# Kernel optimization log

Measured on AMD Instinct MI355X. Metric: run time of the kernel, lower is better.

## Reference

```python
import jax, jax.numpy as jnp
import numpy as np

N = 50000     # num_nodes
E = 600000    # num_edges
H = 128       # h_dim
OUT = 32      # out_dim
R = 64        # num_rels
B = 16        # num_bases


def setup_inputs() -> dict:
    key = jax.random.key(0)
    ks = jax.random.split(key, 11)
    src = jax.random.randint(ks[0], (E,), 0, N)
    dst = jax.random.randint(ks[1], (E,), 0, N)
    etype = jax.random.randint(ks[2], (E,), 0, R)
    norm = jax.random.uniform(ks[3], (E, 1), dtype=jnp.float32)  # edge norm (e.g. 1/deg)
    emb = jax.random.normal(ks[4], (N, H), dtype=jnp.float32) * 0.05
    # basis-decomposed relation weights: W_r = sum_b comp[r,b] * V[b]
    V1 = jax.random.normal(ks[5], (B, H, H), dtype=jnp.float32) * (1.0 / np.sqrt(H))
    comp1 = jax.random.normal(ks[6], (R, B), dtype=jnp.float32) * (1.0 / np.sqrt(B))
    bias1 = jnp.zeros((H,), dtype=jnp.float32)
    V2 = jax.random.normal(ks[7], (B, H, OUT), dtype=jnp.float32) * (1.0 / np.sqrt(H))
    comp2 = jax.random.normal(ks[8], (R, B), dtype=jnp.float32) * (1.0 / np.sqrt(B))
    bias2 = jnp.zeros((OUT,), dtype=jnp.float32)
    return {"src": src, "dst": dst, "etype": etype, "norm": norm, "emb": emb,
            "V1": V1, "comp1": comp1, "bias1": bias1,
            "V2": V2, "comp2": comp2, "bias2": bias2}


def _rel_graph_conv(x, src, dst, etype, norm, V, comp, bias):
    # message for edge e: (x[src_e] @ W_{etype_e}) * norm_e, W_r = sum_b comp[r,b] V_b.
    # Since W is linear, fold norm into the gathered features, and aggregate
    # per (dst, basis) BEFORE the dense basis matmul (aggregate-first trick):
    #   agg[v, b] = sum_{e: dst_e=v} comp[etype_e, b] * norm_e * x[src_e]
    #   out[v]    = sum_b agg[v, b] @ V_b + bias
    xs = x[src] * norm                      # [E, in]
    w = comp[etype]                         # [E, B] per-edge basis coefficients
    # loop over the small fixed basis count (B=16), reusing the [E, in] buffer
    agg = jnp.stack(
        [jax.ops.segment_sum(xs * w[:, b:b + 1], dst, num_segments=N) for b in range(B)],
        axis=1,
    )                                       # [N, B, in]
    return jnp.einsum('nbi,bio->no', agg, V) + bias


def reference(src, dst, etype, norm, emb, V1, comp1, bias1, V2, comp2, bias2):
    h = _rel_graph_conv(emb, src, dst, etype, norm, V1, comp1, bias1)
    h = jax.nn.relu(h)                      # dropout p=0.0 -> identity
    h = _rel_graph_conv(h, src, dst, etype, norm, V2, comp2, bias2)
    return h
```

## Files before the change

### kernel.cpp

```cpp
#include <hip/hip_runtime.h>
#include <hip/hip_bf16.h>

#define NN 50000
#define EE 600000
#define HH 128
#define OUTD 32
#define RR 64
#define BB 16
#define KK 2048
#define SC_B ((NN + 1023) / 1024)

typedef short s16x8 __attribute__((ext_vector_type(8)));
typedef float f32x4 __attribute__((ext_vector_type(4)));
typedef float f32x2 __attribute__((ext_vector_type(2)));
typedef unsigned short ushort_t;
typedef unsigned int uint_t;
typedef __attribute__((address_space(3))) uint_t lds_u32;
typedef const __attribute__((address_space(1))) uint_t glb_u32;

__device__ inline ushort_t f_to_bf16(float f){
    __hip_bfloat16 h = __float2bfloat16(f);
    return *reinterpret_cast<ushort_t*>(&h);
}
__device__ inline uint_t pack_bf16x2(float a, float b){
    return (uint_t)f_to_bf16(a) | ((uint_t)f_to_bf16(b) << 16);
}

__global__ void zero_i32(int* p, int n){
    int i = blockIdx.x*256 + threadIdx.x;
    if (i < n) p[i] = 0;
}

__global__ void hist_kernel(const int* __restrict__ dst, int* counts){
    int e = blockIdx.x*256 + threadIdx.x;
    if (e < EE) atomicAdd(&counts[dst[e]], 1);
}

__global__ void scan_part(const int* __restrict__ counts, int* __restrict__ tot){
    int b = blockIdx.x, t = threadIdx.x;
    int i0 = b*1024 + t*4;
    int s = 0;
    if (i0 + 3 < NN){
        int4 v = *reinterpret_cast<const int4*>(&counts[i0]);
        s = v.x + v.y + v.z + v.w;
    } else {
        for (int j = 0; j < 4; j++) if (i0 + j < NN) s += counts[i0 + j];
    }
    #pragma unroll
    for (int off = 32; off; off >>= 1) s += __shfl_xor(s, off, 64);
    __shared__ int ws[4];
    if ((t & 63) == 0) ws[t >> 6] = s;
    __syncthreads();
    if (t == 0) tot[b] = ws[0] + ws[1] + ws[2] + ws[3];
}

__global__ void scan_tot(int* tot){
    int t = threadIdx.x;
    int v = (t < SC_B) ? tot[t] : 0;
    int x = v;
    #pragma unroll
    for (int off = 1; off < 64; off <<= 1){
        int y = __shfl_up(x, off, 64);
        if (t >= off) x += y;
    }
    if (t < SC_B) tot[t] = x - v;
}

__global__ void scan_final(const int* __restrict__ counts, const int* __restrict__ tot,
                           int* __restrict__ offsets, int* __restrict__ cursor){
    int b = blockIdx.x, t = threadIdx.x, lane = t & 63, wv = t >> 6;
    int i0 = b*1024 + t*4;
    int v[4]; int s = 0;
    #pragma unroll
    for (int j = 0; j < 4; j++){ v[j] = (i0 + j < NN) ? counts[i0 + j] : 0; s += v[j]; }
    int x = s;
    #pragma unroll
    for (int off = 1; off < 64; off <<= 1){
        int y = __shfl_up(x, off, 64);
        if (lane >= off) x += y;
    }
    __shared__ int ws[4];
    if (lane == 63) ws[wv] = x;
    __syncthreads();
    int pre = tot[b];
    for (int i = 0; i < wv; i++) pre += ws[i];
    int run = pre + x - s;
    #pragma unroll
    for (int j = 0; j < 4; j++){
        if (i0 + j < NN){
            cursor[i0 + j] = run;
            offsets[i0 + j + 1] = run + v[j];
        }
        run += v[j];
    }
    if (b == 0 && t == 0) offsets[0] = 0;
}

__global__ void scatter_kernel(const int* __restrict__ dst, const int* __restrict__ src,
                               const int* __restrict__ etype, const float* __restrict__ norm,
                               int* cursor, int* __restrict__ msrc, int* __restrict__ netn){
    int e = blockIdx.x*256 + threadIdx.x;
    if (e >= EE) return;
    int d = dst[e];
    int r = atomicAdd(&cursor[d], 1);
    msrc[r] = src[e];
    netn[r] = (__float_as_int(norm[e]) & ~63) | etype[e];
}

__global__ void convw_kernel(const float* __restrict__ V1, const float* __restrict__ V2,
                             ushort_t* __restrict__ Wt1, ushort_t* __restrict__ Wt2){
    int i = blockIdx.x*256 + threadIdx.x;
    if (i < HH*KK){
        int o = i / KK, k = i % KK;
        Wt1[i] = f_to_bf16(V1[(size_t)k*HH + o]);
    } else {
        int j = i - HH*KK;
        if (j < OUTD*KK){
            int o = j / KK, k = j % KK;
            Wt2[j] = f_to_bf16(V2[(size_t)k*OUTD + o]);
        }
    }
}

__global__ void conv_emb(const float* __restrict__ emb, ushort_t* __restrict__ xb){
    int i = blockIdx.x*256 + threadIdx.x;
    if (i < NN*HH/2){
        float2 f = *reinterpret_cast<const float2*>(emb + 2*(size_t)i);
        *reinterpret_cast<uint_t*>(xb + 2*(size_t)i) = pack_bf16x2(f.x, f.y);
    }
}

__global__ __launch_bounds__(256, 8) void agg_kernel(
    const ushort_t* __restrict__ xin, const int* __restrict__ msrc,
    const int* __restrict__ netn, const int* __restrict__ offsets,
    const float* __restrict__ comp, ushort_t* __restrict__ agg,
    int v0, int vc)
{
    int w = threadIdx.x >> 6, lane = threadIdx.x & 63;
    int v = v0 + blockIdx.x*4 + w;
    if (v >= v0 + vc) return;
    int p0 = offsets[v];
    int dd = offsets[v+1] - p0;
    const uint_t* xrow = reinterpret_cast<const uint_t*>(xin);

    f32x2 accA[8], accB[8];
    #pragma unroll
    for (int bp = 0; bp < 8; bp++){
        accA[bp].x = 0.f; accA[bp].y = 0.f;
        accB[bp].x = 0.f; accB[bp].y = 0.f;
    }

    for (int c0 = 0; c0 < dd; c0 += 64){
        int nc = min(64, dd - c0);
        int li = p0 + c0 + min(lane, nc - 1);
        int mp = msrc[li];
        int nr = netn[li];
        uint_t xr[8];
        #pragma unroll
        for (int j = 0; j < 8; ++j){
            int sr = __builtin_amdgcn_readlane(mp, min(j, nc - 1));
            xr[j] = xrow[(size_t)sr*64 + lane];
        }
        for (int eb = 0; eb < nc; eb += 8){
            #pragma unroll
            for (int j = 0; j < 8; ++j){
                int e = eb + j;
                int ec = min(e, nc - 1);
                int nb = __builtin_amdgcn_readlane(nr, ec);
                int et = nb & 63;
                float nw = (e < nc) ? __int_as_float(nb & ~63) : 0.f;
                uint_t u = xr[j];
                f32x2 xs;
                xs.x = __uint_as_float(u << 16) * nw;
                xs.y = __uint_as_float(u & 0xffff0000u) * nw;
                int en = e + 8;
                if (en < nc){
                    int srn = __builtin_amdgcn_readlane(mp, en);
                    xr[j] = xrow[(size_t)srn*64 + lane];
                }
                const f32x2* cp = reinterpret_cast<const f32x2*>(comp + et*BB);
                #pragma unroll
                for (int bp = 0; bp < 8; bp++){
                    f32x2 c2 = cp[bp];
                    asm("v_pk_fma_f32 %0, %1, %2, %0 op_sel:[0,0,0] op_sel_hi:[1,0,1]"
                        : "+v"(accA[bp]) : "s"(c2), "v"(xs));
                    asm("v_pk_fma_f32 %0, %1, %2, %0 op_sel:[0,1,0] op_sel_hi:[1,1,1]"
                        : "+v"(accB[bp]) : "s"(c2), "v"(xs));
                }
            }
        }
    }
    uint_t* arow = reinterpret_cast<uint_t*>(agg) + (size_t)(v - v0)*1024 + lane;
    #pragma unroll
    for (int b = 0; b < BB; b++)
        arow[b*64] = pack_bf16x2(accA[b>>1][b&1], accB[b>>1][b&1]);
}

template<int BN, bool RELU, bool OUT_BF16>
__global__ __launch_bounds__(512, 4) void gemm_kernel(
    const ushort_t* __restrict__ A, const ushort_t* __restrict__ Wt,
    const float* __restrict__ bias, void* __restrict__ yout, int vc)
{
    __shared__ __align__(16) char Ald[2][128*128];
    __shared__ __align__(16) char Bld[2][BN*128];
    constexpr int RT = (BN == 128) ? 2 : 1;
    constexpr int CT = (BN == 128) ? 4 : 2;
    constexpr int NT = KK / 64;
    int tid = threadIdx.x, lane = tid & 63, lane15 = lane & 15;
    int w = tid >> 6;
    int wrbase = (BN == 128) ? (w >> 1)*32 : w*16;
    int wcbase = (BN == 128) ? (w & 1)*64 : 0;
    int m0 = blockIdx.x * 128;

    int rl = lane >> 3, jl = lane & 7;
    int ra0 = w*2*8 + rl,  ra1 = (w*2+1)*8 + rl;
    const ushort_t* agp0 = A + (size_t)(m0 + min(ra0, vc-1))*KK + ((jl ^ (ra0 & 7))*8);
    const ushort_t* agp1 = A + (size_t)(m0 + min(ra1, vc-1))*KK + ((jl ^ (ra1 & 7))*8);
    const ushort_t* bgp0;
    const ushort_t* bgp1;
    if (BN == 128){
        bgp0 = Wt + (size_t)ra0*KK + ((jl ^ (ra0 & 7))*8);
        bgp1 = Wt + (size_t)ra1*KK + ((jl ^ (ra1 & 7))*8);
    } else {
        int rb = w*8 + rl;
        bgp0 = Wt + (size_t)min(rb, BN-1)*KK + ((jl ^ (rb & 7))*8);
        bgp1 = nullptr;
    }

    auto stage = [&](int buf){
        __builtin_amdgcn_global_load_lds((glb_u32*)agp0,
            (lds_u32*)(&Ald[buf][(w*2+0)*1024]), 16, 0, 0);
        __builtin_amdgcn_global_load_lds((glb_u32*)agp1,
            (lds_u32*)(&Ald[buf][(w*2+1)*1024]), 16, 0, 0);
        agp0 += 64; agp1 += 64;
        if constexpr (BN == 128){
            __builtin_amdgcn_global_load_lds((glb_u32*)bgp0,
                (lds_u32*)(&Bld[buf][(w*2+0)*1024]), 16, 0, 0);
            __builtin_amdgcn_global_load_lds((glb_u32*)bgp1,
                (lds_u32*)(&Bld[buf][(w*2+1)*1024]), 16, 0, 0);
            bgp0 += 64; bgp1 += 64;
        } else {
            if (w < 4){
                __builtin_amdgcn_global_load_lds((glb_u32*)bgp0,
                    (lds_u32*)(&Bld[buf][w*1024]), 16, 0, 0);
                bgp0 += 64;
            }
        }
    };

    f32x4 acc[RT][CT];
    #pragma unroll
    for (int t = 0; t < RT; t++)
        #pragma unroll
        for (int ct = 0; ct < CT; ct++)
            #pragma unroll
            for (int j = 0; j < 4; j++) acc[t][ct][j] = 0.f;

    auto compute = [&](int buf){
        #pragma unroll
        for (int ks = 0; ks < 2; ks++){
            int csw = (ks*4 + (lane >> 4)) ^ (lane15 & 7);
            #pragma unroll
            for (int t = 0; t < RT; t++){
                int arow = wrbase + t*16 + lane15;
                s16x8 a = *reinterpret_cast<const s16x8*>(&Ald[buf][arow*128 + csw*16]);
                #pragma unroll
                for (int ct = 0; ct < CT; ct++){
                    int brow = wcbase + ct*16 + lane15;
                    s16x8 b = *reinterpret_cast<const s16x8*>(&Bld[buf][brow*128 + csw*16]);
                    acc[t][ct] = __builtin_amdgcn_mfma_f32_16x16x32_bf16(a, b, acc[t][ct], 0,0,0);
                }
            }
        }
    };

    stage(0);
    for (int t = 0; t < NT; ++t){
        int cur = t & 1;
        if (t + 1 < NT){
            stage(cur ^ 1);
            if (BN == 128)       asm volatile("s_waitcnt vmcnt(4)" ::: "memory");
            else if (w < 4)      asm volatile("s_waitcnt vmcnt(3)" ::: "memory");
            else                 asm volatile("s_waitcnt vmcnt(2)" ::: "memory");
        } else {
            asm volatile("s_waitcnt vmcnt(0)" ::: "memory");
        }
        __builtin_amdgcn_s_barrier();
        __builtin_amdgcn_sched_barrier(0);
        compute(cur);
        __builtin_amdgcn_s_barrier();
    }

    #pragma unroll
    for (int t = 0; t < RT; t++){
        int rb = m0 + wrbase + t*16 + ((lane >> 4) << 2);
        #pragma unroll
        for (int ct = 0; ct < CT; ct++){
            int col = wcbase + ct*16 + lane15;
            float bv = bias[col];
            #pragma unroll
            for (int r = 0; r < 4; r++){
                int row = rb + r;
                if (row < vc){
                    float val = acc[t][ct][r] + bv;
                    if (RELU) val = fmaxf(val, 0.f);
                    if (OUT_BF16)
                        reinterpret_cast<ushort_t*>(yout)[(size_t)row*BN + col] = f_to_bf16(val);
                    else
                        reinterpret_cast<float*>(yout)[(size_t)row*BN + col] = val;
                }
            }
        }
    }
}

extern "C" void kernel_launch(void* const* d_in, const int* in_sizes, int n_in,
                              void* d_out, int out_size, void* d_ws, size_t ws_size,
                              hipStream_t stream){
    const int*   src   = (const int*)d_in[0];
    const int*   dst   = (const int*)d_in[1];
    const int*   etype = (const int*)d_in[2];
    const float* norm  = (const float*)d_in[3];
    const float* emb   = (const float*)d_in[4];
    const float* V1    = (const float*)d_in[5];
    const float* comp1 = (const float*)d_in[6];
    const float* bias1 = (const float*)d_in[7];
    const float* V2    = (const float*)d_in[8];
    const float* comp2 = (const float*)d_in[9];
    const float* bias2 = (const float*)d_in[10];
    float* out = (float*)d_out;

    char* w = (char*)d_ws;
    auto alloc = [&](size_t bytes) -> char* {
        char* p = w; w += (bytes + 255) & ~(size_t)255; return p;
    };
    int*      offsets = (int*)alloc((NN + 1) * 4);
    int*      counts  = (int*)alloc(NN * 4);
    int*      cursor  = (int*)alloc(NN * 4);
    int*      tot     = (int*)alloc(SC_B * 4);
    int*      msrc    = (int*)alloc((size_t)EE * 4);
    int*      netn    = (int*)alloc((size_t)EE * 4);
    ushort_t* Wt1     = (ushort_t*)alloc((size_t)HH * KK * 2);
    ushort_t* Wt2     = (ushort_t*)alloc((size_t)OUTD * KK * 2);
    ushort_t* xb      = (ushort_t*)alloc((size_t)NN * HH * 2);
    ushort_t* h       = (ushort_t*)alloc((size_t)NN * HH * 2);
    size_t used  = (size_t)(w - (char*)d_ws);
    size_t avail = ws_size > used ? ws_size - used : 0;
    int chunkN = (int)(avail / ((size_t)KK * 2));
    chunkN &= ~127;
    if (chunkN < 128) chunkN = 128;
    if (chunkN > NN) chunkN = NN;
    ushort_t* agg = (ushort_t*)w;

    zero_i32<<<(NN + 255)/256, 256, 0, stream>>>(counts, NN);
    hist_kernel<<<(EE + 255)/256, 256, 0, stream>>>(dst, counts);
    scan_part<<<SC_B, 256, 0, stream>>>(counts, tot);
    scan_tot<<<1, 64, 0, stream>>>(tot);
    scan_final<<<SC_B, 256, 0, stream>>>(counts, tot, offsets, cursor);
    scatter_kernel<<<(EE + 255)/256, 256, 0, stream>>>(dst, src, etype, norm,
                                                       cursor, msrc, netn);
    convw_kernel<<<((HH + OUTD)*KK + 255)/256, 256, 0, stream>>>(V1, V2, Wt1, Wt2);
    conv_emb<<<(NN*HH/2 + 255)/256, 256, 0, stream>>>(emb, xb);

    for (int v0 = 0; v0 < NN; v0 += chunkN){
        int vc = (NN - v0 < chunkN) ? (NN - v0) : chunkN;
        agg_kernel<<<(vc + 3)/4, 256, 0, stream>>>(
            xb, msrc, netn, offsets, comp1, agg, v0, vc);
        gemm_kernel<HH, true, true><<<(vc + 127)/128, 512, 0, stream>>>(
            agg, Wt1, bias1, h + (size_t)v0 * HH, vc);
    }
    for (int v0 = 0; v0 < NN; v0 += chunkN){
        int vc = (NN - v0 < chunkN) ? (NN - v0) : chunkN;
        agg_kernel<<<(vc + 3)/4, 256, 0, stream>>>(
            h, msrc, netn, offsets, comp2, agg, v0, vc);
        gemm_kernel<OUTD, false, false><<<(vc + 127)/128, 512, 0, stream>>>(
            agg, Wt2, bias2, out + (size_t)v0 * OUTD, vc);
    }
}
```

Baseline: 310.1 us.

## Precompute per-edge norm-scaled basis coefficients and fuse prep kernels

Adds a per-edge array wedge[E,16] holding comp[etype]*norm, built in a fused prep kernel for layer 1 and by a separate kernel for layer 2. The aggregation kernel then reads these coefficients directly, dropping the per-edge readlane decode, the etype lookup and the norm multiply, and splits off a tail loop for the last partial group of 8 edges. It also merges the weight and embedding conversion launches into one kernel and replaces the zeroing kernel with hipMemsetAsync. The cost is about 38 MB of extra writes per layer and 64 bytes of coefficient reads per edge instead of a 4-byte packed word.

```diff
diff --git a/kernel.cpp b/kernel.cpp
--- a/kernel.cpp
+++ b/kernel.cpp
@@ -9,6 +9,8 @@
 #define BB 16
 #define KK 2048
 #define SC_B ((NN + 1023) / 1024)
+#define N_CONVW ((HH + OUTD) * KK)
+#define N_EMB   (NN * HH / 2)
 
 typedef short s16x8 __attribute__((ext_vector_type(8)));
 typedef float f32x4 __attribute__((ext_vector_type(4)));
@@ -24,11 +26,6 @@
 }
 __device__ inline uint_t pack_bf16x2(float a, float b){
     return (uint_t)f_to_bf16(a) | ((uint_t)f_to_bf16(b) << 16);
-}
-
-__global__ void zero_i32(int* p, int n){
-    int i = blockIdx.x*256 + threadIdx.x;
-    if (i < n) p[i] = 0;
 }
 
 __global__ void hist_kernel(const int* __restrict__ dst, int* counts){
@@ -107,34 +104,54 @@
     netn[r] = (__float_as_int(norm[e]) & ~63) | etype[e];
 }
 
-__global__ void convw_kernel(const float* __restrict__ V1, const float* __restrict__ V2,
-                             ushort_t* __restrict__ Wt1, ushort_t* __restrict__ Wt2){
+__device__ inline void build_w_one(int e, const int* __restrict__ netn,
+                                   const float* __restrict__ comp,
+                                   float* __restrict__ wedge){
+    int nb = netn[e];
+    int et = nb & 63;
+    float nw = __int_as_float(nb & ~63);
+    const float4* c = reinterpret_cast<const float4*>(comp + et*BB);
+    float4* wp = reinterpret_cast<float4*>(wedge + (size_t)e*BB);
+    #pragma unroll
+    for (int q = 0; q < 4; q++){
+        float4 cv = c[q];
+        wp[q] = make_float4(cv.x*nw, cv.y*nw, cv.z*nw, cv.w*nw);
+    }
+}
+
+__global__ void build_w_kernel(const int* __restrict__ netn, const float* __restrict__ comp,
+                               float* __restrict__ wedge){
+    int e = blockIdx.x*256 + threadIdx.x;
+    if (e < EE) build_w_one(e, netn, comp, wedge);
+}
+
+__global__ void prep_kernel(const float* __restrict__ V1, const float* __restrict__ V2,
+                            const float* __restrict__ emb, const int* __restrict__ netn,
+                            const float* __restrict__ comp1,
+                            ushort_t* __restrict__ Wt1, ushort_t* __restrict__ Wt2,
+                            ushort_t* __restrict__ xb, float* __restrict__ wedge){
     int i = blockIdx.x*256 + threadIdx.x;
     if (i < HH*KK){
         int o = i / KK, k = i % KK;
         Wt1[i] = f_to_bf16(V1[(size_t)k*HH + o]);
+    } else if (i < N_CONVW){
+        int j = i - HH*KK;
+        int o = j / KK, k = j % KK;
+        Wt2[j] = f_to_bf16(V2[(size_t)k*OUTD + o]);
+    } else if (i < N_CONVW + N_EMB){
+        int j = i - N_CONVW;
+        float2 f = *reinterpret_cast<const float2*>(emb + 2*(size_t)j);
+        *reinterpret_cast<uint_t*>(xb + 2*(size_t)j) = pack_bf16x2(f.x, f.y);
     } else {
-        int j = i - HH*KK;
-        if (j < OUTD*KK){
-            int o = j / KK, k = j % KK;
-            Wt2[j] = f_to_bf16(V2[(size_t)k*OUTD + o]);
-        }
-    }
-}
-
-__global__ void conv_emb(const float* __restrict__ emb, ushort_t* __restrict__ xb){
-    int i = blockIdx.x*256 + threadIdx.x;
-    if (i < NN*HH/2){
-        float2 f = *reinterpret_cast<const float2*>(emb + 2*(size_t)i);
-        *reinterpret_cast<uint_t*>(xb + 2*(size_t)i) = pack_bf16x2(f.x, f.y);
+        int e = i - N_CONVW - N_EMB;
+        if (e < EE) build_w_one(e, netn, comp1, wedge);
     }
 }
 
 __global__ __launch_bounds__(256, 8) void agg_kernel(
     const ushort_t* __restrict__ xin, const int* __restrict__ msrc,
-    const int* __restrict__ netn, const int* __restrict__ offsets,
-    const float* __restrict__ comp, ushort_t* __restrict__ agg,
-    int v0, int vc)
+    const float* __restrict__ wedge, const int* __restrict__ offsets,
+    ushort_t* __restrict__ agg, int v0, int vc)
 {
     int w = threadIdx.x >> 6, lane = threadIdx.x & 63;
     int v = v0 + blockIdx.x*4 + w;
@@ -152,33 +169,49 @@
 
     for (int c0 = 0; c0 < dd; c0 += 64){
         int nc = min(64, dd - c0);
-        int li = p0 + c0 + min(lane, nc - 1);
-        int mp = msrc[li];
-        int nr = netn[li];
+        int sp = __builtin_amdgcn_readfirstlane(p0 + c0);
+        int mp = msrc[sp + min(lane, nc - 1)];
         uint_t xr[8];
         #pragma unroll
         for (int j = 0; j < 8; ++j){
             int sr = __builtin_amdgcn_readlane(mp, min(j, nc - 1));
             xr[j] = xrow[(size_t)sr*64 + lane];
         }
-        for (int eb = 0; eb < nc; eb += 8){
+        const f32x2* wb = reinterpret_cast<const f32x2*>(wedge) + (size_t)sp*8;
+        int ebf = nc & ~7;
+        for (int eb = 0; eb < ebf; eb += 8){
             #pragma unroll
             for (int j = 0; j < 8; ++j){
                 int e = eb + j;
-                int ec = min(e, nc - 1);
-                int nb = __builtin_amdgcn_readlane(nr, ec);
-                int et = nb & 63;
-                float nw = (e < nc) ? __int_as_float(nb & ~63) : 0.f;
                 uint_t u = xr[j];
                 f32x2 xs;
-                xs.x = __uint_as_float(u << 16) * nw;
-                xs.y = __uint_as_float(u & 0xffff0000u) * nw;
+                xs.x = __uint_as_float(u << 16);
+                xs.y = __uint_as_float(u & 0xffff0000u);
                 int en = e + 8;
                 if (en < nc){
                     int srn = __builtin_amdgcn_readlane(mp, en);
                     xr[j] = xrow[(size_t)srn*64 + lane];
                 }
-                const f32x2* cp = reinterpret_cast<const f32x2*>(comp + et*BB);
+                const f32x2* cp = wb + (size_t)e*8;
+                #pragma unroll
+                for (int bp = 0; bp < 8; bp++){
+                    f32x2 c2 = cp[bp];
+                    asm("v_pk_fma_f32 %0, %1, %2, %0 op_sel:[0,0,0] op_sel_hi:[1,0,1]"
+                        : "+v"(accA[bp]) : "s"(c2), "v"(xs));
+                    asm("v_pk_fma_f32 %0, %1, %2, %0 op_sel:[0,1,0] op_sel_hi:[1,1,1]"
+                        : "+v"(accB[bp]) : "s"(c2), "v"(xs));
+                }
+            }
+        }
+        #pragma unroll
+        for (int j = 0; j < 8; ++j){
+            int e = ebf + j;
+            if (e < nc){
+                uint_t u = xr[j];
+                f32x2 xs;
+                xs.x = __uint_as_float(u << 16);
+                xs.y = __uint_as_float(u & 0xffff0000u);
+                const f32x2* cp = wb + (size_t)e*8;
                 #pragma unroll
                 for (int bp = 0; bp < 8; bp++){
                     f32x2 c2 = cp[bp];
@@ -340,6 +373,7 @@
     int*      tot     = (int*)alloc(SC_B * 4);
     int*      msrc    = (int*)alloc((size_t)EE * 4);
     int*      netn    = (int*)alloc((size_t)EE * 4);
+    float*    wedge   = (float*)alloc((size_t)EE * BB * 4);
     ushort_t* Wt1     = (ushort_t*)alloc((size_t)HH * KK * 2);
     ushort_t* Wt2     = (ushort_t*)alloc((size_t)OUTD * KK * 2);
     ushort_t* xb      = (ushort_t*)alloc((size_t)NN * HH * 2);
@@ -352,27 +386,28 @@
     if (chunkN > NN) chunkN = NN;
     ushort_t* agg = (ushort_t*)w;
 
-    zero_i32<<<(NN + 255)/256, 256, 0, stream>>>(counts, NN);
+    hipMemsetAsync(counts, 0, NN * 4, stream);
     hist_kernel<<<(EE + 255)/256, 256, 0, stream>>>(dst, counts);
     scan_part<<<SC_B, 256, 0, stream>>>(counts, tot);
     scan_tot<<<1, 64, 0, stream>>>(tot);
     scan_final<<<SC_B, 256, 0, stream>>>(counts, tot, offsets, cursor);
     scatter_kernel<<<(EE + 255)/256, 256, 0, stream>>>(dst, src, etype, norm,
                                                        cursor, msrc, netn);
-    convw_kernel<<<((HH + OUTD)*KK + 255)/256, 256, 0, stream>>>(V1, V2, Wt1, Wt2);
-    conv_emb<<<(NN*HH/2 + 255)/256, 256, 0, stream>>>(emb, xb);
+    prep_kernel<<<(N_CONVW + N_EMB + EE + 255)/256, 256, 0, stream>>>(
+        V1, V2, emb, netn, comp1, Wt1, Wt2, xb, wedge);
 
     for (int v0 = 0; v0 < NN; v0 += chunkN){
         int vc = (NN - v0 < chunkN) ? (NN - v0) : chunkN;
         agg_kernel<<<(vc + 3)/4, 256, 0, stream>>>(
-            xb, msrc, netn, offsets, comp1, agg, v0, vc);
+            xb, msrc, wedge, offsets, agg, v0, vc);
         gemm_kernel<HH, true, true><<<(vc + 127)/128, 512, 0, stream>>>(
             agg, Wt1, bias1, h + (size_t)v0 * HH, vc);
     }
+    build_w_kernel<<<(EE + 255)/256, 256, 0, stream>>>(netn, comp2, wedge);
     for (int v0 = 0; v0 < NN; v0 += chunkN){
         int vc = (NN - v0 < chunkN) ? (NN - v0) : chunkN;
         agg_kernel<<<(vc + 3)/4, 256, 0, stream>>>(
-            h, msrc, netn, offsets, comp2, agg, v0, vc);
+            h, msrc, wedge, offsets, agg, v0, vc);
         gemm_kernel<OUTD, false, false><<<(vc + 127)/128, 512, 0, stream>>>(
             agg, Wt2, bias2, out + (size_t)v0 * OUTD, vc);
     }
```

Measured after the change: 461.2 us. 48.7% more time.
